# Performance work log

Hardware: AMD Instinct MI355X
Metric: run time of the kernel (lower is better)

The kernel has to match this reference:

```python
import jax, jax.numpy as jnp
import numpy as np
from jax import lax

N, CIN, H, W = 128, 1024, 14, 14
CF, TH = 128, 128          # cv_filter, te_hidden
HP, GT, FP, A = 256, 256, 256, 32


def setup_inputs() -> dict:
    key = jax.random.key(0)
    ks = jax.random.split(key, 12)
    s = 0.05
    return {
        "image": jax.random.normal(ks[0], (N, CIN, H, W), jnp.float32),
        "code": jax.random.normal(ks[1], (N, TH), jnp.float32),
        "conv_w": jax.random.normal(ks[2], (CF, CIN, 3, 3), jnp.float32) * 0.02,
        "conv_b": jnp.zeros((CF,), jnp.float32),
        "hp_w0": jax.random.normal(ks[3], (CF + 2 + TH, HP), jnp.float32) * s,
        "hp_b0": jnp.zeros((HP,), jnp.float32),
        "hp_w1": jax.random.normal(ks[4], (HP, 1), jnp.float32) * s,
        "hp_b1": jnp.zeros((1,), jnp.float32),
        "gt_w0": jax.random.normal(ks[5], ((CF + 2) * 2 + TH, GT), jnp.float32) * s,
        "gt_b0": jnp.zeros((GT,), jnp.float32),
        "gt_w1": jax.random.normal(ks[6], (GT, GT), jnp.float32) * s,
        "gt_b1": jnp.zeros((GT,), jnp.float32),
        "fp_w0": jax.random.normal(ks[7], (GT, FP), jnp.float32) * s,
        "fp_b0": jnp.zeros((FP,), jnp.float32),
        "fp_w1": jax.random.normal(ks[8], (FP, A), jnp.float32) * s,
        "fp_b1": jnp.zeros((A,), jnp.float32),
    }


def _sarn(image, code, conv_w, conv_b, hp_w0, hp_b0, hp_w1, hp_b1,
          gt_w0, gt_b0, gt_w1, gt_b1, fp_w0, fp_b0, fp_w1, fp_b1):
    # visual_resize: 3x3 conv, stride 1, pad 1 (NCHW)
    x = lax.conv_general_dilated(image, conv_w, (1, 1), "SAME",
                                 dimension_numbers=("NCHW", "OIHW", "NCHW"))
    x = x + conv_b[None, :, None, None]                       # [n, cf, h, w]
    n, c, h, w = x.shape
    o = h * w
    # sarn_encode: append x/y coordinate channels and question code
    xc = jnp.broadcast_to(jnp.linspace(-1.0, 1.0, h).reshape(1, 1, h, 1), (n, 1, h, w))
    yc = jnp.broadcast_to(jnp.linspace(-1.0, 1.0, w).reshape(1, 1, 1, w), (n, 1, h, w))
    coord = jnp.concatenate([x, xc, yc], axis=1)              # [n, cf+2, h, w]
    q = jnp.broadcast_to(code[:, :, None, None], (n, code.shape[1], h, w))
    qenc = jnp.concatenate([coord, q], axis=1)                # [n, cf+2+th, h, w]
    ce = coord.reshape(n, c + 2, o).transpose(0, 2, 1)        # [n, o, cf+2]
    qe = qenc.reshape(n, -1, o).transpose(0, 2, 1)            # [n, o, cf+2+th]
    # h_psi: per-object attention logit
    a = jax.nn.relu(jnp.einsum("nod,dh->noh", qe, hp_w0) + hp_b0)
    att = jnp.einsum("noh,hk->nok", a, hp_w1) + hp_b1         # [n, o, 1]
    # sarn_pair: softmax select a single soft object, pair with every object
    sel = jax.nn.softmax(att[..., 0], axis=1)                 # [n, o]
    selected = jnp.einsum("no,nod->nd", sel, ce)              # [n, cf+2]
    pairs = jnp.concatenate(
        [qe, jnp.broadcast_to(selected[:, None, :], ce.shape)], axis=2)  # [n, o, 2*(cf+2)+th]
    # g_theta MLP + sum over objects
    g = jax.nn.relu(jnp.einsum("nop,pg->nog", pairs, gt_w0) + gt_b0)
    g = jax.nn.relu(jnp.einsum("nog,gk->nok", g, gt_w1) + gt_b1)
    relations = g.sum(axis=1)                                 # [n, gt]
    # f_phi MLP -> answer logits
    f = jax.nn.relu(relations @ fp_w0 + fp_b0)
    return f @ fp_w1 + fp_b1                                  # [n, a_size]


def reference(image, code, conv_w, conv_b, hp_w0, hp_b0, hp_w1, hp_b1,
              gt_w0, gt_b0, gt_w1, gt_b1, fp_w0, fp_b0, fp_w1, fp_b1):
    return _sarn(image, code, conv_w, conv_b, hp_w0, hp_b0, hp_w1, hp_b1,
                 gt_w0, gt_b0, gt_w1, gt_b1, fp_w0, fp_b0, fp_w1, fp_b1)
```

## Files before the change

kernel.cpp:

```cpp
#include <hip/hip_runtime.h>
#include <stdint.h>

typedef unsigned short u16;
typedef __bf16 bf16x8 __attribute__((ext_vector_type(8)));
typedef float f32x4 __attribute__((ext_vector_type(4)));

__device__ __forceinline__ u16 f2b(float f) {
  union { float f; uint32_t u; } v; v.f = f;
  uint32_t r = v.u + 0x7fffu + ((v.u >> 16) & 1u);
  return (u16)(r >> 16);
}
__device__ __forceinline__ float b2f(u16 b) {
  union { float f; uint32_t u; } v; v.u = ((uint32_t)b) << 16;
  return v.f;
}
__device__ __forceinline__ void g2l16(const void* g, void* l) {
  __builtin_amdgcn_global_load_lds(
      (const __attribute__((address_space(1))) void*)g,
      (__attribute__((address_space(3))) void*)l, 16, 0, 0);
}

#define N_SAMP 128
#define OPAD   224
#define ROWS   (N_SAMP * OPAD)

__global__ __launch_bounds__(256) void prep_weights(
    const float* __restrict__ conv_w, const float* __restrict__ hp_w0,
    const float* __restrict__ gt_w0, const float* __restrict__ gt_w1,
    u16* __restrict__ W2, u16* __restrict__ hp_w0t,
    u16* __restrict__ gt_w0t, u16* __restrict__ gt_w1t) {
  int idx = blockIdx.x * 256 + threadIdx.x;
  const int nW2 = 9 * 128 * 1024;
  const int nHP = 256 * 288;
  const int nGT0 = 256 * 288;
  const int nGT1 = 256 * 256;
  if (idx < nW2) {
    int s = idx / 131072; int r = idx & 131071;
    int cf = r >> 10; int cin = r & 1023;
    W2[idx] = f2b(conv_w[(cf * 1024 + cin) * 9 + s]);
    return;
  }
  idx -= nW2;
  if (idx < nHP) {
    int nn = idx / 288, kk = idx % 288;
    hp_w0t[nn * 288 + kk] = (kk < 258) ? f2b(hp_w0[kk * 256 + nn]) : (u16)0;
    return;
  }
  idx -= nHP;
  if (idx < nGT0) {
    int nn = idx / 288, kk = idx % 288;
    gt_w0t[nn * 288 + kk] = (kk < 258) ? f2b(gt_w0[kk * 256 + nn]) : (u16)0;
    return;
  }
  idx -= nGT0;
  if (idx < nGT1) {
    int nn = idx >> 8, kk = idx & 255;
    gt_w1t[nn * 256 + kk] = f2b(gt_w1[kk * 256 + nn]);
  }
}

__global__ __launch_bounds__(256) void prep_img(const float* __restrict__ image,
                                                u16* __restrict__ imgT) {
  __shared__ float t[64][197];
  int n = blockIdx.x >> 4;
  int cin0 = (blockIdx.x & 15) * 64;
  const float* src = image + ((size_t)n * 1024 + cin0) * 196;
  for (int e = threadIdx.x; e < 64 * 196; e += 256) {
    int c = e / 196, sp = e % 196;
    t[c][sp] = src[c * 196 + sp];
  }
  __syncthreads();
  int w = threadIdx.x >> 6, lane = threadIdx.x & 63;
  for (int i = 0; i < 64; ++i) {
    int spg = i * 4 + w;
    int gy = spg >> 4, gx = spg & 15;
    float v = 0.f;
    if (gy >= 1 && gy <= 14 && gx >= 1 && gx <= 14) v = t[lane][(gy - 1) * 14 + (gx - 1)];
    imgT[(((size_t)(n * 256 + spg)) << 10) + cin0 + lane] = f2b(v);
  }
}

__global__ __launch_bounds__(256) void fill_qe(const float* __restrict__ code,
                                               u16* __restrict__ qeb) {
  int base = blockIdx.x * 8;
  for (int rr = 0; rr < 8; ++rr) {
    int r = base + rr;
    int n = r / 224, o = r % 224;
    int y = o / 14, x = o % 14;
    bool valid = o < 196;
    u16* row = qeb + (size_t)r * 288;
    for (int c = threadIdx.x; c < 288; c += 256) {
      u16 v;
      if (c < 128) { if (valid) continue; v = 0; }
      else if (c == 128) v = valid ? f2b(-1.f + 2.f * y / 13.f) : (u16)0;
      else if (c == 129) v = valid ? f2b(-1.f + 2.f * x / 13.f) : (u16)0;
      else if (c < 258) v = valid ? f2b(code[n * 128 + (c - 130)]) : (u16)0;
      else v = 0;
      row[c] = v;
    }
  }
}

__global__ __launch_bounds__(256) void conv_gemm(
    const u16* __restrict__ imgT, const u16* __restrict__ W2,
    float* __restrict__ convAcc) {
  __shared__ __align__(16) u16 lA[112 * 64];
  __shared__ __align__(16) u16 lB[128 * 64];
  int tid = threadIdx.x, lane = tid & 63, w = tid >> 6;
  int wg = blockIdx.x;
  int xcd = wg & 7, grp = wg >> 3;
  int n = ((grp / 6) << 3) | xcd;
  int r6 = grp % 6;
  int oh = r6 / 3, ks = r6 % 3;
  int oBase = oh * 112;
  size_t nBase = (size_t)n << 8;
  int rowIn = lane >> 3;
  int cA = ((lane & 7) ^ rowIn) << 3;

  int yxA[4];
  for (int ii = 0; ii < 4; ++ii) {
    int t = w + ii * 4;
    int o = oBase + t * 8 + rowIn;
    bool valid = o < 196;
    int y = o / 14, x = o - y * 14;
    yxA[ii] = valid ? (y * 16 + x) : 0;
  }

  f32x4 acc[7][2];
#pragma unroll
  for (int mt = 0; mt < 7; ++mt)
#pragma unroll
    for (int j = 0; j < 2; ++j) acc[mt][j] = (f32x4){0.f, 0.f, 0.f, 0.f};

  int l = lane & 15, q = lane >> 4;
  for (int si = 0; si < 3; ++si) {
    int s = ks * 3 + si;
    int off = (s / 3) * 16 + (s % 3);
    const u16* Ws = W2 + ((size_t)(s * 128) << 10);
    for (int cb = 0; cb < 16; ++cb) {
      int k0 = cb << 6;
      __syncthreads();
      g2l16(imgT + ((nBase + (size_t)(yxA[0] + off)) << 10) + k0 + cA, &lA[(w) * 512]);
      g2l16(imgT + ((nBase + (size_t)(yxA[1] + off)) << 10) + k0 + cA, &lA[(w + 4) * 512]);
      g2l16(imgT + ((nBase + (size_t)(yxA[2] + off)) << 10) + k0 + cA, &lA[(w + 8) * 512]);
      if (w < 2)
        g2l16(imgT + ((nBase + (size_t)(yxA[3] + off)) << 10) + k0 + cA, &lA[(w + 12) * 512]);
#pragma unroll
      for (int ii = 0; ii < 4; ++ii) {
        int t = w + ii * 4;
        g2l16(Ws + ((size_t)(t * 8 + rowIn) << 10) + k0 + cA, &lB[t * 512]);
      }
      __syncthreads();
#pragma unroll
      for (int kk = 0; kk < 2; ++kk) {
        int co = ((((kk << 2) | q) ^ (l & 7)) << 3);
        bf16x8 af[7];
#pragma unroll
        for (int mt = 0; mt < 7; ++mt)
          af[mt] = *(const bf16x8*)&lA[(mt * 16 + l) * 64 + co];
#pragma unroll
        for (int jj = 0; jj < 2; ++jj) {
          bf16x8 bb = *(const bf16x8*)&lB[(w * 32 + jj * 16 + l) * 64 + co];
#pragma unroll
          for (int mt = 0; mt < 7; ++mt)
            acc[mt][jj] = __builtin_amdgcn_mfma_f32_16x16x32_bf16(af[mt], bb, acc[mt][jj], 0, 0, 0);
        }
      }
    }
  }
#pragma unroll
  for (int mt = 0; mt < 7; ++mt) {
    int o = oBase + mt * 16 + q * 4;
#pragma unroll
    for (int r4 = 0; r4 < 4; ++r4) {
      if (o + r4 < 196) {
        float* dst = convAcc + (size_t)(n * 224 + o + r4) * 128 + w * 32 + l;
        atomicAdd(dst, acc[mt][0][r4]);
        atomicAdd(dst + 16, acc[mt][1][r4]);
      }
    }
  }
}

__global__ __launch_bounds__(256) void conv_fix(
    const float* __restrict__ convAcc, const float* __restrict__ conv_b,
    u16* __restrict__ qeb) {
  int idx = blockIdx.x * 256 + threadIdx.x;
  int row196 = idx >> 5;
  int c0 = (idx & 31) << 2;
  int n = row196 / 196, o = row196 - n * 196;
  size_t row = (size_t)(n * 224 + o);
  const float4 v = *(const float4*)(convAcc + (row << 7) + c0);
  const float4 b = *(const float4*)(conv_b + c0);
  ushort4 pk;
  pk.x = f2b(v.x + b.x); pk.y = f2b(v.y + b.y);
  pk.z = f2b(v.z + b.z); pk.w = f2b(v.w + b.w);
  *(ushort4*)(qeb + row * 288 + c0) = pk;
}

template <int MODE, int KP, int KC>
__global__ __launch_bounds__(256) void gemm_kernel(
    const u16* __restrict__ A, const u16* __restrict__ Bt,
    const float* __restrict__ bias, const float* __restrict__ vec,
    float* __restrict__ outF, u16* __restrict__ outB) {
  __shared__ __align__(16) u16 lA[112 * 32];
  __shared__ __align__(16) u16 lB[128 * 32];
  int tid = threadIdx.x, lane = tid & 63, w = tid >> 6;
  int bx = blockIdx.x, by = blockIdx.y;
  int r0 = bx * 112;
  int cBase = by * 128;
  int kb = (((lane & 3) ^ ((lane >> 3) & 3)) << 3);
  int rA0 = r0 + w * 16 + (lane >> 2);
  int rA1 = r0 + (w + 4) * 16 + (lane >> 2);
  bool has1 = (w < 3);
  const u16* gA0 = A + (size_t)rA0 * KP + kb;
  const u16* gA1 = A + (size_t)rA1 * KP + kb;
  int cB0 = cBase + w * 16 + (lane >> 2);
  int cB1 = cBase + (w + 4) * 16 + (lane >> 2);
  const u16* gB0 = Bt + (size_t)cB0 * KP + kb;
  const u16* gB1 = Bt + (size_t)cB1 * KP + kb;

  f32x4 acc[7][2];
#pragma unroll
  for (int mt = 0; mt < 7; ++mt)
#pragma unroll
    for (int j = 0; j < 2; ++j) acc[mt][j] = (f32x4){0.f, 0.f, 0.f, 0.f};
  int colW = w * 32;
  int l = lane & 15, q = lane >> 4;
  int co = ((q ^ ((l >> 1) & 3)) << 3);

  for (int cb = 0; cb < KC; ++cb) {
    __syncthreads();
    g2l16(gA0 + cb * 32, &lA[w * 512]);
    if (has1) g2l16(gA1 + cb * 32, &lA[(w + 4) * 512]);
    g2l16(gB0 + cb * 32, &lB[w * 512]);
    g2l16(gB1 + cb * 32, &lB[(w + 4) * 512]);
    __syncthreads();
    bf16x8 af[7];
#pragma unroll
    for (int mt = 0; mt < 7; ++mt)
      af[mt] = *(const bf16x8*)&lA[(mt * 16 + l) * 32 + co];
#pragma unroll
    for (int j = 0; j < 2; ++j) {
      bf16x8 bfr = *(const bf16x8*)&lB[(colW + j * 16 + l) * 32 + co];
#pragma unroll
      for (int mt = 0; mt < 7; ++mt)
        acc[mt][j] = __builtin_amdgcn_mfma_f32_16x16x32_bf16(af[mt], bfr, acc[mt][j], 0, 0, 0);
    }
  }

  int q4 = lane >> 4, c = lane & 15;
  if (MODE == 0) {
    float attp[7][4];
#pragma unroll
    for (int mt = 0; mt < 7; ++mt)
#pragma unroll
      for (int r = 0; r < 4; ++r) attp[mt][r] = 0.f;
#pragma unroll
    for (int j = 0; j < 2; ++j) {
      int col = cBase + colW + j * 16 + c;
      float b0 = bias[col], w1 = vec[col];
#pragma unroll
      for (int mt = 0; mt < 7; ++mt)
#pragma unroll
        for (int r = 0; r < 4; ++r) {
          float v = fmaxf(acc[mt][j][r] + b0, 0.f);
          attp[mt][r] += v * w1;
        }
    }
#pragma unroll
    for (int mt = 0; mt < 7; ++mt)
#pragma unroll
      for (int r = 0; r < 4; ++r) {
        float p = attp[mt][r];
        p += __shfl_xor(p, 1, 64);
        p += __shfl_xor(p, 2, 64);
        p += __shfl_xor(p, 4, 64);
        p += __shfl_xor(p, 8, 64);
        if (c == 0) atomicAdd(&outF[r0 + mt * 16 + q4 * 4 + r], p);
      }
  } else if (MODE == 1) {
    int n = bx >> 1;
#pragma unroll
    for (int mt = 0; mt < 7; ++mt)
#pragma unroll
      for (int j = 0; j < 2; ++j) {
        int col = cBase + colW + j * 16 + c;
        float b = bias[n * 256 + col];
#pragma unroll
        for (int r = 0; r < 4; ++r) {
          int row = r0 + mt * 16 + q4 * 4 + r;
          outB[(size_t)row * 256 + col] = f2b(fmaxf(acc[mt][j][r] + b, 0.f));
        }
      }
  } else {
    int n = bx >> 1;
    int ob = (bx & 1) * 112;
#pragma unroll
    for (int j = 0; j < 2; ++j) {
      int col = cBase + colW + j * 16 + c;
      float b = bias[col];
      float sum = 0.f;
#pragma unroll
      for (int mt = 0; mt < 7; ++mt)
#pragma unroll
        for (int r = 0; r < 4; ++r) {
          int o = ob + mt * 16 + q4 * 4 + r;
          if (o < 196) sum += fmaxf(acc[mt][j][r] + b, 0.f);
        }
      sum += __shfl_xor(sum, 16, 64);
      sum += __shfl_xor(sum, 32, 64);
      if (q4 == 0) atomicAdd(&outF[n * 256 + col], sum);
    }
  }
}

__global__ __launch_bounds__(256) void sel_kernel(
    const float* __restrict__ att, const u16* __restrict__ qeb,
    const float* __restrict__ gt_w0, const float* __restrict__ gt_b0,
    float* __restrict__ bias2) {
  int n = blockIdx.x, t = threadIdx.x;
  int w = t >> 6, lane = t & 63;
  __shared__ u16 sq[196][130];
  __shared__ float sm[196];
  __shared__ float sel[130];
  __shared__ float red[8];
  const u16* base = qeb + (size_t)n * 224 * 288;
  for (int o = w; o < 196; o += 4) {
    const u16* rowp = base + (size_t)o * 288;
    for (int c = lane; c < 130; c += 64) sq[o][c] = rowp[c];
  }
  float a = (t < 196) ? att[n * 224 + t] : -1e30f;
  float m = a;
  for (int mask = 1; mask < 64; mask <<= 1) m = fmaxf(m, __shfl_xor(m, mask, 64));
  if (lane == 0) red[w] = m;
  __syncthreads();
  float M = fmaxf(fmaxf(red[0], red[1]), fmaxf(red[2], red[3]));
  float e = (t < 196) ? expf(a - M) : 0.f;
  float sAcc = e;
  for (int mask = 1; mask < 64; mask <<= 1) sAcc += __shfl_xor(sAcc, mask, 64);
  if (lane == 0) red[4 + w] = sAcc;
  __syncthreads();
  float S = red[4] + red[5] + red[6] + red[7];
  if (t < 196) sm[t] = e / S;
  __syncthreads();
  if (t < 130) {
    float acc = 0.f;
    for (int o = 0; o < 196; ++o) acc += sm[o] * b2f(sq[o][t]);
    sel[t] = acc;
  }
  __syncthreads();
  float acc2 = gt_b0[t];
  for (int d = 0; d < 130; ++d) acc2 += sel[d] * gt_w0[(258 + d) * 256 + t];
  bias2[n * 256 + t] = acc2;
}

__global__ __launch_bounds__(256) void fphi(
    const float* __restrict__ relations, const float* __restrict__ fp_w0,
    const float* __restrict__ fp_b0, const float* __restrict__ fp_w1,
    const float* __restrict__ fp_b1, float* __restrict__ out) {
  int n = blockIdx.x, t = threadIdx.x;
  __shared__ float rel[256];
  __shared__ float f[256];
  rel[t] = relations[n * 256 + t];
  __syncthreads();
  float acc = fp_b0[t];
  for (int k = 0; k < 256; ++k) acc += rel[k] * fp_w0[k * 256 + t];
  f[t] = fmaxf(acc, 0.f);
  __syncthreads();
  if (t < 32) {
    float o = fp_b1[0];
    for (int k = 0; k < 256; ++k) o += f[k] * fp_w1[k * 32 + t];
    out[n * 32 + t] = o;
  }
}

extern "C" void kernel_launch(void* const* d_in, const int* in_sizes, int n_in,
                              void* d_out, int out_size, void* d_ws, size_t ws_size,
                              hipStream_t stream) {
  const float* image = (const float*)d_in[0];
  const float* code = (const float*)d_in[1];
  const float* conv_w = (const float*)d_in[2];
  const float* conv_b = (const float*)d_in[3];
  const float* hp_w0 = (const float*)d_in[4];
  const float* hp_b0 = (const float*)d_in[5];
  const float* hp_w1 = (const float*)d_in[6];
  const float* gt_w0 = (const float*)d_in[8];
  const float* gt_b0 = (const float*)d_in[9];
  const float* gt_w1 = (const float*)d_in[10];
  const float* gt_b1 = (const float*)d_in[11];
  const float* fp_w0 = (const float*)d_in[12];
  const float* fp_b0 = (const float*)d_in[13];
  const float* fp_w1 = (const float*)d_in[14];
  const float* fp_b1 = (const float*)d_in[15];
  float* out = (float*)d_out;

  char* p = (char*)d_ws;
  u16* imgT = (u16*)p;   p += (size_t)128 * 256 * 1024 * 2;
  u16* W2 = (u16*)p;     p += (size_t)9 * 128 * 1024 * 2;
  u16* qeb = (u16*)p;    p += (size_t)ROWS * 288 * 2;
  u16* hp_w0t = (u16*)p; p += (size_t)256 * 288 * 2;
  u16* gt_w0t = (u16*)p; p += (size_t)256 * 288 * 2;
  u16* gt_w1t = (u16*)p; p += (size_t)256 * 256 * 2;
  float* att = (float*)p;   p += (size_t)ROWS * 4;
  float* bias2 = (float*)p; p += (size_t)128 * 256 * 4;
  float* convAcc = (float*)p; p += (size_t)ROWS * 128 * 4;
  float* relations = (float*)p; p += (size_t)128 * 256 * 4;
  u16* g1 = (u16*)convAcc;

  hipMemsetAsync(att, 0, (size_t)ROWS * 4, stream);
  hipMemsetAsync(relations, 0, (size_t)128 * 256 * 4, stream);
  hipMemsetAsync(convAcc, 0, (size_t)ROWS * 128 * 4, stream);

  prep_weights<<<5440, 256, 0, stream>>>(conv_w, hp_w0, gt_w0, gt_w1, W2, hp_w0t, gt_w0t, gt_w1t);
  prep_img<<<2048, 256, 0, stream>>>(image, imgT);
  fill_qe<<<ROWS / 8, 256, 0, stream>>>(code, qeb);
  conv_gemm<<<768, 256, 0, stream>>>(imgT, W2, convAcc);
  conv_fix<<<3136, 256, 0, stream>>>(convAcc, conv_b, qeb);
  gemm_kernel<0, 288, 9><<<dim3(256, 2), 256, 0, stream>>>(qeb, hp_w0t, hp_b0, hp_w1, att, nullptr);
  sel_kernel<<<128, 256, 0, stream>>>(att, qeb, gt_w0, gt_b0, bias2);
  gemm_kernel<1, 288, 9><<<dim3(256, 2), 256, 0, stream>>>(qeb, gt_w0t, bias2, nullptr, nullptr, g1);
  gemm_kernel<2, 256, 8><<<dim3(256, 2), 256, 0, stream>>>(g1, gt_w1t, gt_b1, nullptr, relations, nullptr);
  fphi<<<128, 256, 0, stream>>>(relations, fp_w0, fp_b0, fp_w1, fp_b1, out);
}
```

Before: 412.9 us.

## Fuse prep kernels and memsets, restructure conv GEMM split and attention GEMM

Merges the weight prep, qe fill and buffer zeroing into one prep_misc kernel, which removes three memsets and one launch, and makes the conv weight transpose read coalesced through shared memory. The conv GEMM now splits K four ways (1024 blocks), loads the B fragments straight from global into registers instead of LDS, and sets launch bounds for 4 blocks per SM. The attention GEMM becomes a 512-thread kernel that covers all 256 columns per block and reduces through LDS, so global atomics and the att memset are no longer needed. The cost is extra atomic traffic from the finer conv K-split and uncached global B loads in the conv inner loop.

```diff
diff --git a/kernel.cpp b/kernel.cpp
--- a/kernel.cpp
+++ b/kernel.cpp
@@ -4,6 +4,7 @@
 typedef unsigned short u16;
 typedef __bf16 bf16x8 __attribute__((ext_vector_type(8)));
 typedef float f32x4 __attribute__((ext_vector_type(4)));
+typedef unsigned short u16x8 __attribute__((ext_vector_type(8)));
 
 __device__ __forceinline__ u16 f2b(float f) {
   union { float f; uint32_t u; } v; v.f = f;
@@ -24,38 +25,85 @@
 #define OPAD   224
 #define ROWS   (N_SAMP * OPAD)
 
-__global__ __launch_bounds__(256) void prep_weights(
+__global__ __launch_bounds__(256) void prep_misc(
     const float* __restrict__ conv_w, const float* __restrict__ hp_w0,
     const float* __restrict__ gt_w0, const float* __restrict__ gt_w1,
+    const float* __restrict__ code,
     u16* __restrict__ W2, u16* __restrict__ hp_w0t,
-    u16* __restrict__ gt_w0t, u16* __restrict__ gt_w1t) {
-  int idx = blockIdx.x * 256 + threadIdx.x;
-  const int nW2 = 9 * 128 * 1024;
-  const int nHP = 256 * 288;
-  const int nGT0 = 256 * 288;
-  const int nGT1 = 256 * 256;
-  if (idx < nW2) {
-    int s = idx / 131072; int r = idx & 131071;
-    int cf = r >> 10; int cin = r & 1023;
-    W2[idx] = f2b(conv_w[(cf * 1024 + cin) * 9 + s]);
+    u16* __restrict__ gt_w0t, u16* __restrict__ gt_w1t,
+    u16* __restrict__ qeb, float* __restrict__ convAcc,
+    float* __restrict__ relations) {
+  __shared__ float sw[2304];
+  __shared__ u16 tmpl[176];
+  int b = blockIdx.x, tid = threadIdx.x;
+  if (b < 3584) {
+    f32x4 z = {0.f, 0.f, 0.f, 0.f};
+    *(f32x4*)(convAcc + ((size_t)(b * 256 + tid) << 2)) = z;
     return;
   }
-  idx -= nW2;
-  if (idx < nHP) {
-    int nn = idx / 288, kk = idx % 288;
-    hp_w0t[nn * 288 + kk] = (kk < 258) ? f2b(hp_w0[kk * 256 + nn]) : (u16)0;
+  b -= 3584;
+  if (b < 32) {
+    f32x4 z = {0.f, 0.f, 0.f, 0.f};
+    *(f32x4*)(relations + ((size_t)(b * 256 + tid) << 2)) = z;
     return;
   }
-  idx -= nHP;
-  if (idx < nGT0) {
-    int nn = idx / 288, kk = idx % 288;
-    gt_w0t[nn * 288 + kk] = (kk < 258) ? f2b(gt_w0[kk * 256 + nn]) : (u16)0;
+  b -= 32;
+  if (b < 512) {
+    size_t base = (size_t)b * 2304;
+#pragma unroll
+    for (int i = 0; i < 9; ++i) sw[tid + 256 * i] = conv_w[base + tid + 256 * i];
+    __syncthreads();
+    int f = b * 256 + tid;
+    int cf = f >> 10, cin = f & 1023;
+#pragma unroll
+    for (int k = 0; k < 9; ++k)
+      W2[(size_t)k * 131072 + cf * 1024 + cin] = f2b(sw[tid * 9 + k]);
     return;
   }
-  idx -= nGT0;
-  if (idx < nGT1) {
+  b -= 512;
+  if (b < 288) {
+    int idx = b * 256 + tid;
+    int nn = idx / 288, kk = idx - nn * 288;
+    hp_w0t[idx] = (kk < 258) ? f2b(hp_w0[kk * 256 + nn]) : (u16)0;
+    return;
+  }
+  b -= 288;
+  if (b < 288) {
+    int idx = b * 256 + tid;
+    int nn = idx / 288, kk = idx - nn * 288;
+    gt_w0t[idx] = (kk < 258) ? f2b(gt_w0[kk * 256 + nn]) : (u16)0;
+    return;
+  }
+  b -= 288;
+  if (b < 256) {
+    int idx = b * 256 + tid;
     int nn = idx >> 8, kk = idx & 255;
-    gt_w1t[nn * 256 + kk] = f2b(gt_w1[kk * 256 + nn]);
+    gt_w1t[idx] = f2b(gt_w1[kk * 256 + nn]);
+    return;
+  }
+  b -= 256;
+  {
+    int n = b;
+    if (tid < 176) {
+      int c = 128 + tid;
+      u16 v = 0;
+      if (c >= 130 && c < 258) v = f2b(code[n * 128 + c - 130]);
+      tmpl[tid] = v;
+    }
+    __syncthreads();
+    for (int it = 0; it < 16; ++it) {
+      int ch = it * 256 + tid;
+      if (ch < 3920) {
+        int o = ch / 20, j = ch - o * 20;
+        u16x8 v = *(const u16x8*)&tmpl[j * 8];
+        if (j == 0) {
+          int y = o / 14, x = o - y * 14;
+          v[0] = f2b(-1.f + 2.f * y / 13.f);
+          v[1] = f2b(-1.f + 2.f * x / 13.f);
+        }
+        *(u16x8*)(qeb + (size_t)(n * 224 + o) * 288 + 128 + j * 8) = v;
+      }
+    }
   }
 }
 
@@ -80,44 +128,23 @@
   }
 }
 
-__global__ __launch_bounds__(256) void fill_qe(const float* __restrict__ code,
-                                               u16* __restrict__ qeb) {
-  int base = blockIdx.x * 8;
-  for (int rr = 0; rr < 8; ++rr) {
-    int r = base + rr;
-    int n = r / 224, o = r % 224;
-    int y = o / 14, x = o % 14;
-    bool valid = o < 196;
-    u16* row = qeb + (size_t)r * 288;
-    for (int c = threadIdx.x; c < 288; c += 256) {
-      u16 v;
-      if (c < 128) { if (valid) continue; v = 0; }
-      else if (c == 128) v = valid ? f2b(-1.f + 2.f * y / 13.f) : (u16)0;
-      else if (c == 129) v = valid ? f2b(-1.f + 2.f * x / 13.f) : (u16)0;
-      else if (c < 258) v = valid ? f2b(code[n * 128 + (c - 130)]) : (u16)0;
-      else v = 0;
-      row[c] = v;
-    }
-  }
-}
-
-__global__ __launch_bounds__(256) void conv_gemm(
+__global__ __launch_bounds__(256, 4) void conv_gemm(
     const u16* __restrict__ imgT, const u16* __restrict__ W2,
     float* __restrict__ convAcc) {
   __shared__ __align__(16) u16 lA[112 * 64];
-  __shared__ __align__(16) u16 lB[128 * 64];
   int tid = threadIdx.x, lane = tid & 63, w = tid >> 6;
   int wg = blockIdx.x;
   int xcd = wg & 7, grp = wg >> 3;
-  int n = ((grp / 6) << 3) | xcd;
-  int r6 = grp % 6;
-  int oh = r6 / 3, ks = r6 % 3;
+  int nIdx = grp >> 3, r8 = grp & 7;
+  int oh = r8 >> 2, ks = r8 & 3;
+  int n = (nIdx << 3) | xcd;
   int oBase = oh * 112;
   size_t nBase = (size_t)n << 8;
   int rowIn = lane >> 3;
   int cA = ((lane & 7) ^ rowIn) << 3;
 
   int yxA[4];
+#pragma unroll
   for (int ii = 0; ii < 4; ++ii) {
     int t = w + ii * 4;
     int o = oBase + t * 8 + rowIn;
@@ -133,39 +160,39 @@
     for (int j = 0; j < 2; ++j) acc[mt][j] = (f32x4){0.f, 0.f, 0.f, 0.f};
 
   int l = lane & 15, q = lane >> 4;
-  for (int si = 0; si < 3; ++si) {
-    int s = ks * 3 + si;
-    int off = (s / 3) * 16 + (s % 3);
-    const u16* Ws = W2 + ((size_t)(s * 128) << 10);
-    for (int cb = 0; cb < 16; ++cb) {
-      int k0 = cb << 6;
-      __syncthreads();
-      g2l16(imgT + ((nBase + (size_t)(yxA[0] + off)) << 10) + k0 + cA, &lA[(w) * 512]);
-      g2l16(imgT + ((nBase + (size_t)(yxA[1] + off)) << 10) + k0 + cA, &lA[(w + 4) * 512]);
-      g2l16(imgT + ((nBase + (size_t)(yxA[2] + off)) << 10) + k0 + cA, &lA[(w + 8) * 512]);
-      if (w < 2)
-        g2l16(imgT + ((nBase + (size_t)(yxA[3] + off)) << 10) + k0 + cA, &lA[(w + 12) * 512]);
-#pragma unroll
-      for (int ii = 0; ii < 4; ++ii) {
-        int t = w + ii * 4;
-        g2l16(Ws + ((size_t)(t * 8 + rowIn) << 10) + k0 + cA, &lB[t * 512]);
-      }
-      __syncthreads();
-#pragma unroll
-      for (int kk = 0; kk < 2; ++kk) {
-        int co = ((((kk << 2) | q) ^ (l & 7)) << 3);
-        bf16x8 af[7];
-#pragma unroll
-        for (int mt = 0; mt < 7; ++mt)
-          af[mt] = *(const bf16x8*)&lA[(mt * 16 + l) * 64 + co];
-#pragma unroll
-        for (int jj = 0; jj < 2; ++jj) {
-          bf16x8 bb = *(const bf16x8*)&lB[(w * 32 + jj * 16 + l) * 64 + co];
-#pragma unroll
-          for (int mt = 0; mt < 7; ++mt)
-            acc[mt][jj] = __builtin_amdgcn_mfma_f32_16x16x32_bf16(af[mt], bb, acc[mt][jj], 0, 0, 0);
-        }
-      }
+  const u16* Wl = W2 + ((size_t)(w * 32 + l) << 10) + q * 8;
+
+  for (int u = ks * 36; u < ks * 36 + 36; ++u) {
+    int s = u >> 4, cb = u & 15, k0 = cb << 6;
+    int s3 = s / 3;
+    int off = s3 * 16 + (s - s3 * 3);
+    const u16* Wp = Wl + ((size_t)s << 17) + k0;
+    bf16x8 bj0k0 = *(const bf16x8*)(Wp);
+    bf16x8 bj1k0 = *(const bf16x8*)(Wp + (16 << 10));
+    bf16x8 bj0k1 = *(const bf16x8*)(Wp + 32);
+    bf16x8 bj1k1 = *(const bf16x8*)(Wp + (16 << 10) + 32);
+    __syncthreads();
+    g2l16(imgT + ((nBase + (size_t)(yxA[0] + off)) << 10) + k0 + cA, &lA[(w) * 512]);
+    g2l16(imgT + ((nBase + (size_t)(yxA[1] + off)) << 10) + k0 + cA, &lA[(w + 4) * 512]);
+    g2l16(imgT + ((nBase + (size_t)(yxA[2] + off)) << 10) + k0 + cA, &lA[(w + 8) * 512]);
+    if (w < 2)
+      g2l16(imgT + ((nBase + (size_t)(yxA[3] + off)) << 10) + k0 + cA, &lA[(w + 12) * 512]);
+    __syncthreads();
+#pragma unroll
+    for (int kk = 0; kk < 2; ++kk) {
+      int co = ((((kk << 2) | q) ^ (l & 7)) << 3);
+      bf16x8 af[7];
+#pragma unroll
+      for (int mt = 0; mt < 7; ++mt)
+        af[mt] = *(const bf16x8*)&lA[(mt * 16 + l) * 64 + co];
+#pragma unroll
+      for (int mt = 0; mt < 7; ++mt)
+        acc[mt][0] = __builtin_amdgcn_mfma_f32_16x16x32_bf16(af[mt], kk ? bj0k1 : bj0k0,
+                                                             acc[mt][0], 0, 0, 0);
+#pragma unroll
+      for (int mt = 0; mt < 7; ++mt)
+        acc[mt][1] = __builtin_amdgcn_mfma_f32_16x16x32_bf16(af[mt], kk ? bj1k1 : bj1k0,
+                                                             acc[mt][1], 0, 0, 0);
     }
   }
 #pragma unroll
@@ -196,6 +223,87 @@
   pk.x = f2b(v.x + b.x); pk.y = f2b(v.y + b.y);
   pk.z = f2b(v.z + b.z); pk.w = f2b(v.w + b.w);
   *(ushort4*)(qeb + row * 288 + c0) = pk;
+}
+
+__global__ __launch_bounds__(512) void att_kernel(
+    const u16* __restrict__ A, const u16* __restrict__ Bt,
+    const float* __restrict__ bias, const float* __restrict__ vec,
+    float* __restrict__ att) {
+  __shared__ __align__(16) u16 lA[112 * 32];
+  __shared__ __align__(16) u16 lB[256 * 32];
+  __shared__ float attL[112];
+  int tid = threadIdx.x, lane = tid & 63, w = tid >> 6;
+  int r0 = blockIdx.x * 112;
+  if (tid < 112) attL[tid] = 0.f;
+  int kb = (((lane & 3) ^ ((lane >> 3) & 3)) << 3);
+  const u16* gA0 = A + (size_t)(r0 + w * 16 + (lane >> 2)) * 288 + kb;
+  const u16* gA1 = A + (size_t)(r0 + (w + 4) * 16 + (lane >> 2)) * 288 + kb;
+  int wb = w - 4;
+
+  f32x4 acc[7][2];
+#pragma unroll
+  for (int mt = 0; mt < 7; ++mt)
+#pragma unroll
+    for (int j = 0; j < 2; ++j) acc[mt][j] = (f32x4){0.f, 0.f, 0.f, 0.f};
+  int l = lane & 15, q = lane >> 4;
+  int co = ((q ^ ((l >> 1) & 3)) << 3);
+  int colW = w * 32;
+
+  for (int cb = 0; cb < 9; ++cb) {
+    __syncthreads();
+    if (w < 4) {
+      g2l16(gA0 + cb * 32, &lA[w * 512]);
+      if (w < 3) g2l16(gA1 + cb * 32, &lA[(w + 4) * 512]);
+    } else {
+#pragma unroll
+      for (int ii = 0; ii < 4; ++ii) {
+        int g = wb * 4 + ii;
+        g2l16(Bt + (size_t)(g * 16 + (lane >> 2)) * 288 + kb + cb * 32, &lB[g * 512]);
+      }
+    }
+    __syncthreads();
+    bf16x8 af[7];
+#pragma unroll
+    for (int mt = 0; mt < 7; ++mt)
+      af[mt] = *(const bf16x8*)&lA[(mt * 16 + l) * 32 + co];
+#pragma unroll
+    for (int j = 0; j < 2; ++j) {
+      bf16x8 bfr = *(const bf16x8*)&lB[(colW + j * 16 + l) * 32 + co];
+#pragma unroll
+      for (int mt = 0; mt < 7; ++mt)
+        acc[mt][j] = __builtin_amdgcn_mfma_f32_16x16x32_bf16(af[mt], bfr, acc[mt][j], 0, 0, 0);
+    }
+  }
+  float attp[7][4];
+#pragma unroll
+  for (int mt = 0; mt < 7; ++mt)
+#pragma unroll
+    for (int r = 0; r < 4; ++r) attp[mt][r] = 0.f;
+#pragma unroll
+  for (int j = 0; j < 2; ++j) {
+    int col = colW + j * 16 + l;
+    float b0 = bias[col], w1 = vec[col];
+#pragma unroll
+    for (int mt = 0; mt < 7; ++mt)
+#pragma unroll
+      for (int r = 0; r < 4; ++r) {
+        float v = fmaxf(acc[mt][j][r] + b0, 0.f);
+        attp[mt][r] += v * w1;
+      }
+  }
+#pragma unroll
+  for (int mt = 0; mt < 7; ++mt)
+#pragma unroll
+    for (int r = 0; r < 4; ++r) {
+      float p = attp[mt][r];
+      p += __shfl_xor(p, 1, 64);
+      p += __shfl_xor(p, 2, 64);
+      p += __shfl_xor(p, 4, 64);
+      p += __shfl_xor(p, 8, 64);
+      if (l == 0) atomicAdd(&attL[mt * 16 + q * 4 + r], p);
+    }
+  __syncthreads();
+  if (tid < 112) att[r0 + tid] = attL[tid];
 }
 
 template <int MODE, int KP, int KC>
@@ -250,36 +358,7 @@
   }
 
   int q4 = lane >> 4, c = lane & 15;
-  if (MODE == 0) {
-    float attp[7][4];
-#pragma unroll
-    for (int mt = 0; mt < 7; ++mt)
-#pragma unroll
-      for (int r = 0; r < 4; ++r) attp[mt][r] = 0.f;
-#pragma unroll
-    for (int j = 0; j < 2; ++j) {
-      int col = cBase + colW + j * 16 + c;
-      float b0 = bias[col], w1 = vec[col];
-#pragma unroll
-      for (int mt = 0; mt < 7; ++mt)
-#pragma unroll
-        for (int r = 0; r < 4; ++r) {
-          float v = fmaxf(acc[mt][j][r] + b0, 0.f);
-          attp[mt][r] += v * w1;
-        }
-    }
-#pragma unroll
-    for (int mt = 0; mt < 7; ++mt)
-#pragma unroll
-      for (int r = 0; r < 4; ++r) {
-        float p = attp[mt][r];
-        p += __shfl_xor(p, 1, 64);
-        p += __shfl_xor(p, 2, 64);
-        p += __shfl_xor(p, 4, 64);
-        p += __shfl_xor(p, 8, 64);
-        if (c == 0) atomicAdd(&outF[r0 + mt * 16 + q4 * 4 + r], p);
-      }
-  } else if (MODE == 1) {
+  if (MODE == 1) {
     int n = bx >> 1;
 #pragma unroll
     for (int mt = 0; mt < 7; ++mt)
@@ -408,16 +487,12 @@
   float* relations = (float*)p; p += (size_t)128 * 256 * 4;
   u16* g1 = (u16*)convAcc;
 
-  hipMemsetAsync(att, 0, (size_t)ROWS * 4, stream);
-  hipMemsetAsync(relations, 0, (size_t)128 * 256 * 4, stream);
-  hipMemsetAsync(convAcc, 0, (size_t)ROWS * 128 * 4, stream);
-
-  prep_weights<<<5440, 256, 0, stream>>>(conv_w, hp_w0, gt_w0, gt_w1, W2, hp_w0t, gt_w0t, gt_w1t);
+  prep_misc<<<5088, 256, 0, stream>>>(conv_w, hp_w0, gt_w0, gt_w1, code,
+                                      W2, hp_w0t, gt_w0t, gt_w1t, qeb, convAcc, relations);
   prep_img<<<2048, 256, 0, stream>>>(image, imgT);
-  fill_qe<<<ROWS / 8, 256, 0, stream>>>(code, qeb);
-  conv_gemm<<<768, 256, 0, stream>>>(imgT, W2, convAcc);
+  conv_gemm<<<1024, 256, 0, stream>>>(imgT, W2, convAcc);
   conv_fix<<<3136, 256, 0, stream>>>(convAcc, conv_b, qeb);
-  gemm_kernel<0, 288, 9><<<dim3(256, 2), 256, 0, stream>>>(qeb, hp_w0t, hp_b0, hp_w1, att, nullptr);
+  att_kernel<<<256, 512, 0, stream>>>(qeb, hp_w0t, hp_b0, hp_w1, att);
   sel_kernel<<<128, 256, 0, stream>>>(att, qeb, gt_w0, gt_b0, bias2);
   gemm_kernel<1, 288, 9><<<dim3(256, 2), 256, 0, stream>>>(qeb, gt_w0t, bias2, nullptr, nullptr, g1);
   gemm_kernel<2, 256, 8><<<dim3(256, 2), 256, 0, stream>>>(g1, gt_w1t, gt_b1, nullptr, relations, nullptr);
```

Result: no change. 420.7 us (+1.9%).
